# Performance work log

Hardware: AMD Instinct MI355X
Metric: run time of the kernel (lower is better)

The kernel has to match this reference:

```python
import jax, jax.numpy as jnp
import numpy as np

N = 10000
E = 160000
B = 16
NEG_SLOPE = 0.2


def gat_conv(x, src, dst, W, a_src, a_dst, b, heads, ch):
    # x: [N, F_in]; src/dst: [E'] (self-loops included); W: [F_in, heads*ch]
    n = x.shape[0]
    h = (x @ W).reshape(n, heads, ch)                     # [N,H,C]
    alpha_src = jnp.sum(h * a_src, axis=-1)               # [N,H]
    alpha_dst = jnp.sum(h * a_dst, axis=-1)               # [N,H]
    e = jax.nn.leaky_relu(alpha_src[src] + alpha_dst[dst], NEG_SLOPE)  # [E,H]
    # segment softmax over edges grouped by destination node
    m = jax.ops.segment_max(e, dst, num_segments=n)       # [N,H]
    ex = jnp.exp(e - m[dst])                              # [E,H]
    denom = jax.ops.segment_sum(ex, dst, num_segments=n)  # [N,H]
    alpha = ex / denom[dst]                               # [E,H]
    out = jax.ops.segment_sum(alpha[:, :, None] * h[src], dst, num_segments=n)  # [N,H,C]
    return out.reshape(n, heads * ch) + b


def setup_inputs() -> dict:
    key = jax.random.key(0)
    ks = jax.random.split(key, 16)
    glorot = lambda k, shp: jax.random.normal(k, shp, jnp.float32) * np.sqrt(2.0 / (shp[0] + shp[-1]))
    inp = {
        "x": jax.random.normal(ks[0], (N, 128), jnp.float32),
        "edge_index": jax.random.randint(ks[1], (2, E), 0, N, jnp.int64),
        "batch": jnp.sort(jax.random.randint(ks[2], (N,), 0, B, jnp.int64)),
        # conv1: 128 -> 128 per head, 8 heads
        "W1": glorot(ks[3], (128, 8 * 128)),
        "att_src1": glorot(ks[4], (8, 128)),
        "att_dst1": glorot(ks[5], (8, 128)),
        "b1": jnp.zeros((8 * 128,), jnp.float32),
        # conv2: 1024 -> 64 per head, 8 heads
        "W2": glorot(ks[6], (1024, 8 * 64)),
        "att_src2": glorot(ks[7], (8, 64)),
        "att_dst2": glorot(ks[8], (8, 64)),
        "b2": jnp.zeros((8 * 64,), jnp.float32),
        "fc1_w": glorot(ks[9], (512, 32)),
        "fc1_b": jnp.zeros((32,), jnp.float32),
        "fc2_w": glorot(ks[10], (32, 10)),
        "fc2_b": jnp.zeros((10,), jnp.float32),
    }
    return inp


def reference(x, edge_index, batch, W1, att_src1, att_dst1, b1,
              W2, att_src2, att_dst2, b2, fc1_w, fc1_b, fc2_w, fc2_b):
    n = x.shape[0]
    loop = jnp.arange(n, dtype=edge_index.dtype)
    src = jnp.concatenate([edge_index[0], loop])  # PyG add_self_loops=True
    dst = jnp.concatenate([edge_index[1], loop])
    h = jax.nn.elu(gat_conv(x, src, dst, W1, att_src1, att_dst1, b1, 8, 128))   # [N,1024]
    h = jax.nn.elu(gat_conv(h, src, dst, W2, att_src2, att_dst2, b2, 8, 64))    # [N,512]
    # global mean pool over graphs
    sums = jax.ops.segment_sum(h, batch, num_segments=B)                        # [B,512]
    cnt = jax.ops.segment_sum(jnp.ones((n,), h.dtype), batch, num_segments=B)
    g = sums / jnp.maximum(cnt, 1.0)[:, None]
    g = jax.nn.elu(g @ fc1_w + fc1_b)
    return g @ fc2_w + fc2_b                                                    # [B,10]
```

## Files before the change

kernel.cpp:

```cpp
#include <hip/hip_runtime.h>
#include <math.h>

#define HEADS 8
#define NEG 0.2f

typedef unsigned short ushort_t;
typedef __attribute__((ext_vector_type(8))) short short8;
typedef float f32x4 __attribute__((ext_vector_type(4)));

__device__ inline ushort_t f2bf(float f) {
  union { float f; unsigned u; } v; v.f = f;
  unsigned r = (v.u + 0x7FFF + ((v.u >> 16) & 1)) >> 16;
  return (ushort_t)r;
}

__device__ inline float4 bf4(uint2 v) {
  union { unsigned u; float f; } a, b, c, d;
  a.u = v.x << 16; b.u = v.x & 0xffff0000u;
  c.u = v.y << 16; d.u = v.y & 0xffff0000u;
  return make_float4(a.f, b.f, c.f, d.f);
}

__device__ inline float elu_f(float v) {
  return (v > 0.f) ? v : (__expf(v) - 1.f);
}

#define GLDS16(gp, lp)                                                          \
  __builtin_amdgcn_global_load_lds(                                             \
      (const __attribute__((address_space(1))) void*)(gp),                      \
      (__attribute__((address_space(3))) void*)(lp), 16, 0, 0)

__global__ __launch_bounds__(256) void init_k(int* __restrict__ ws, int zero_words,
                                              const float* __restrict__ x,
                                              ushort_t* __restrict__ xb,
                                              const float* __restrict__ W1,
                                              ushort_t* __restrict__ w1t,
                                              const float* __restrict__ W2,
                                              ushort_t* __restrict__ w2t,
                                              const float* __restrict__ as1,
                                              const float* __restrict__ ad1,
                                              float* __restrict__ Ps,
                                              float* __restrict__ Pd, int nx4) {
  __shared__ float tile[32][33];
  int blk = blockIdx.x;
  if (blk < 640) {
    const float* W; ushort_t* Wt; int K, N, tk, tn;
    if (blk < 128) { W = W1; Wt = w1t; K = 128; N = 1024; tk = blk >> 5; tn = blk & 31; }
    else { W = W2; Wt = w2t; K = 1024; N = 512; int t = blk - 128; tk = t >> 4; tn = t & 15; }
    int tx = threadIdx.x & 31, ty = threadIdx.x >> 5;
    int k0 = tk * 32, n0 = tn * 32;
#pragma unroll
    for (int r = 0; r < 4; r++)
      tile[ty + r * 8][tx] = W[(size_t)(k0 + ty + r * 8) * N + n0 + tx];
    __syncthreads();
#pragma unroll
    for (int r = 0; r < 4; r++)
      Wt[(size_t)(n0 + ty + r * 8) * K + k0 + tx] = f2bf(tile[tx][ty + r * 8]);
  } else if (blk < 648) {
    int h = blk - 640;
    int t = threadIdx.x;
    int k = t >> 1, sd = t & 1;
    const float* att = sd ? ad1 : as1;
    float* P = sd ? Pd : Ps;
    const float* wrow = &W1[(size_t)k * 1024 + h * 128];
    const float* arow = &att[h * 128];
    float s = 0.f;
#pragma unroll 8
    for (int c = 0; c < 128; c++) s += wrow[c] * arow[c];
    P[k * 8 + h] = s;
  } else {
    int i = (blk - 648) * 256 + threadIdx.x;
    if (i < zero_words) ws[i] = 0;
    if (i < nx4) {
      float4 v = ((const float4*)x)[i];
      ushort_t o[4] = {f2bf(v.x), f2bf(v.y), f2bf(v.z), f2bf(v.w)};
      *(uint2*)&xb[i * 4] = *(uint2*)o;
    }
  }
}

__global__ void prep_k(const int* __restrict__ ei, int* __restrict__ src,
                       int* __restrict__ dst, int* __restrict__ deg,
                       const int* __restrict__ batch, int* __restrict__ bstart,
                       int* __restrict__ bend, int E, int Nn) {
  int i = blockIdx.x * blockDim.x + threadIdx.x;
  if (i < Nn) {
    int b = batch[i];
    if (i == 0 || batch[i - 1] != b) bstart[b] = i;
    if (i == Nn - 1 || batch[i + 1] != b) bend[b] = i + 1;
  }
  if (i >= E + Nn) return;
  int s, d;
  if (i < E) { s = ei[i]; d = ei[E + i]; }
  else       { s = d = i - E; }
  src[i] = s;
  dst[i] = d;
  atomicAdd(&deg[d], 1);
}

__global__ __launch_bounds__(1024) void scan_k(const int* __restrict__ deg,
                                               int* __restrict__ offs,
                                               int* __restrict__ cursor, int Nn) {
  __shared__ int wtot[16];
  __shared__ int wexcl[16];
  __shared__ int soff_s;
  int t = threadIdx.x;
  int lane = t & 63, w = t >> 6;
  if (t == 0) soff_s = 0;
  __syncthreads();
  for (int base = 0; base < Nn; base += 4096) {
    int idx = base + 4 * t;
    int4 v = make_int4(0, 0, 0, 0);
    if (idx + 3 < Nn) v = *(const int4*)&deg[idx];
    else {
      if (idx < Nn)     v.x = deg[idx];
      if (idx + 1 < Nn) v.y = deg[idx + 1];
      if (idx + 2 < Nn) v.z = deg[idx + 2];
      if (idx + 3 < Nn) v.w = deg[idx + 3];
    }
    int s1 = v.x, s2 = s1 + v.y, s3 = s2 + v.z, s4 = s3 + v.w;
    int sc = s4;
#pragma unroll
    for (int o = 1; o < 64; o <<= 1) {
      int x = __shfl_up(sc, o);
      if (lane >= o) sc += x;
    }
    if (lane == 63) wtot[w] = sc;
    __syncthreads();
    if (w == 0) {
      int tv = (lane < 16) ? wtot[lane] : 0;
      int ts = tv;
#pragma unroll
      for (int o = 1; o < 16; o <<= 1) {
        int x = __shfl_up(ts, o);
        if (lane >= o) ts += x;
      }
      if (lane < 16) wexcl[lane] = ts - tv;
      if (lane == 15) wtot[15] = ts;
    }
    __syncthreads();
    int excl = soff_s + wexcl[w] + (sc - s4);
    int o0 = excl, o1 = excl + s1, o2 = excl + s2, o3 = excl + s3;
    if (idx < Nn)     { offs[idx] = o0;     cursor[idx] = o0; }
    if (idx + 1 < Nn) { offs[idx + 1] = o1; cursor[idx + 1] = o1; }
    if (idx + 2 < Nn) { offs[idx + 2] = o2; cursor[idx + 2] = o2; }
    if (idx + 3 < Nn) { offs[idx + 3] = o3; cursor[idx + 3] = o3; }
    int chunk_total = wtot[15];
    __syncthreads();
    if (t == 0) soff_s += chunk_total;
    __syncthreads();
  }
  if (t == 0) offs[Nn] = soff_s;
}

__global__ __launch_bounds__(256) void scatter_k(const int* __restrict__ src,
                                                 const int* __restrict__ dst,
                                                 int* __restrict__ cursor,
                                                 int* __restrict__ psrc, int Etot, int eb,
                                                 const float* __restrict__ x,
                                                 const float* __restrict__ Ps,
                                                 const float* __restrict__ Pd,
                                                 float* __restrict__ asrc,
                                                 float* __restrict__ adst, int Nn) {
  if ((int)blockIdx.x >= eb) {
    __shared__ float ps[1024], pd[1024];
    int t = threadIdx.x;
    for (int i = t; i < 1024; i += 256) { ps[i] = Ps[i]; pd[i] = Pd[i]; }
    __syncthreads();
    int n = (blockIdx.x - eb) * 256 + t;
    if (n >= Nn) return;
    const float4* xr = (const float4*)&x[(size_t)n * 128];
    float as[8], ad[8];
#pragma unroll
    for (int h = 0; h < 8; h++) { as[h] = 0.f; ad[h] = 0.f; }
    for (int k4 = 0; k4 < 32; k4++) {
      float4 xv = xr[k4];
      float xs[4] = {xv.x, xv.y, xv.z, xv.w};
#pragma unroll
      for (int j = 0; j < 4; j++) {
        int k = k4 * 4 + j;
#pragma unroll
        for (int h = 0; h < 8; h++) {
          as[h] += xs[j] * ps[k * 8 + h];
          ad[h] += xs[j] * pd[k * 8 + h];
        }
      }
    }
#pragma unroll
    for (int h = 0; h < 8; h++) {
      asrc[n * 8 + h] = as[h];
      adst[n * 8 + h] = ad[h];
    }
    return;
  }
  int i = blockIdx.x * 256 + threadIdx.x;
  if (i >= Etot) return;
  int p = atomicAdd(&cursor[dst[i]], 1);
  psrc[p] = src[i];
}

__global__ __launch_bounds__(64) void aggx_k(const ushort_t* __restrict__ xb,
                                             const float* __restrict__ asrc,
                                             const float* __restrict__ adst,
                                             const int* __restrict__ offs,
                                             const int* __restrict__ psrc,
                                             ushort_t* __restrict__ sb, int Nn) {
  int n = blockIdx.x;
  int l = threadIdx.x;
  int u_mine = l >> 3, h_mine = l & 7;
  float adn = adst[n * 8 + h_mine];
  int e0 = offs[n], e1 = offs[n + 1];
  int c0 = l * 2;
  float acc0[8], acc1[8], wsum[8];
#pragma unroll
  for (int h = 0; h < 8; h++) { acc0[h] = 0.f; acc1[h] = 0.f; wsum[h] = 0.f; }

  for (int i = e0; i < e1; i += 8) {
    int bs = min(8, e1 - i);
    int eu = i + (u_mine < bs ? u_mine : bs - 1);
    int se = psrc[eu];
    float v = asrc[se * 8 + h_mine] + adn;
    v = (v > 0.f) ? v : NEG * v;
    float wm = __expf(v);
    int ss[8];
    unsigned xvv[8];
#pragma unroll
    for (int u = 0; u < 8; u++) ss[u] = psrc[i + (u < bs ? u : bs - 1)];
#pragma unroll
    for (int u = 0; u < 8; u++) xvv[u] = *(const unsigned*)&xb[(size_t)ss[u] * 128 + c0];
#pragma unroll
    for (int u = 0; u < 8; u++) {
      if (u < bs) {
        union { unsigned u; float f; } a, b;
        a.u = xvv[u] << 16; b.u = xvv[u] & 0xffff0000u;
#pragma unroll
        for (int h = 0; h < 8; h++) {
          float w = __shfl(wm, (u << 3) | h);
          acc0[h] += w * a.f;
          acc1[h] += w * b.f;
          wsum[h] += w;
        }
      }
    }
  }

#pragma unroll
  for (int h = 0; h < 8; h++) {
    float inv = 1.f / wsum[h];
    unsigned pr = (unsigned)f2bf(acc0[h] * inv) | ((unsigned)f2bf(acc1[h] * inv) << 16);
    *(unsigned*)&sb[(size_t)n * 1024 + h * 128 + c0] = pr;
  }
}

__global__ __launch_bounds__(256) void hgemm_k(const ushort_t* __restrict__ S,
                                               const ushort_t* __restrict__ Wt,
                                               const float* __restrict__ bias,
                                               ushort_t* __restrict__ G, int M) {
  __shared__ __attribute__((aligned(16))) ushort_t lds[32768];
  int tid = threadIdx.x;
  int lane = tid & 63;
  int wave = tid >> 6;
  int wm = (wave >> 1) * 64, wn = (wave & 1) * 64;
  int head = blockIdx.x;
  int hb0 = head * 128;
  int bm = blockIdx.y * 128;
  int lrow = lane & 15, lq = lane >> 4;

  f32x4 acc[4][4];
#pragma unroll
  for (int i = 0; i < 4; i++)
#pragma unroll
    for (int j = 0; j < 4; j++) acc[i][j] = 0.f;

  int srow = lane >> 3;
  int scol = 8 * ((lane & 7) ^ srow);
  const ushort_t* pa[4];
  const ushort_t* pb[4];
  int lofs[4];
#pragma unroll
  for (int c = 0; c < 4; c++) {
    int row = wave * 32 + c * 8 + srow;
    int ga = min(bm + row, M - 1);
    pa[c] = &S[(size_t)ga * 1024 + hb0 + scol];
    pb[c] = &Wt[(size_t)(hb0 + row) * 128 + scol];
    lofs[c] = (wave * 4 + c) * 512;
  }

  auto stage = [&](int buf, int k0) {
#pragma unroll
    for (int c = 0; c < 4; c++) GLDS16(pa[c] + k0, &lds[buf * 8192 + lofs[c]]);
#pragma unroll
    for (int c = 0; c < 4; c++) GLDS16(pb[c] + k0, &lds[16384 + buf * 8192 + lofs[c]]);
  };
  auto compute = [&](int buf) {
    const ushort_t* Asb = &lds[buf * 8192];
    const ushort_t* Bsb = &lds[16384 + buf * 8192];
#pragma unroll
    for (int ks = 0; ks < 2; ks++) {
      short8 af[4], bfr[4];
#pragma unroll
      for (int t = 0; t < 4; t++) {
        int cbs = (ks * 64 + lq * 16) ^ ((lrow & 7) << 4);
        af[t]  = *(const short8*)&Asb[(wm + t * 16 + lrow) * 64 + (cbs >> 1)];
        bfr[t] = *(const short8*)&Bsb[(wn + t * 16 + lrow) * 64 + (cbs >> 1)];
      }
#pragma unroll
      for (int i = 0; i < 4; i++)
#pragma unroll
        for (int j = 0; j < 4; j++)
          acc[i][j] = __builtin_amdgcn_mfma_f32_16x16x32_bf16(af[i], bfr[j], acc[i][j], 0, 0, 0);
    }
  };

  stage(0, 0);
  asm volatile("s_waitcnt vmcnt(0)" ::: "memory");
  __builtin_amdgcn_s_barrier();
  stage(1, 64);
  compute(0);
  asm volatile("s_waitcnt vmcnt(0)" ::: "memory");
  __builtin_amdgcn_s_barrier();
  compute(1);

  __syncthreads();

  ushort_t* Cl = lds;
  float bv[4];
#pragma unroll
  for (int j = 0; j < 4; j++) bv[j] = bias[hb0 + wn + j * 16 + lrow];
#pragma unroll
  for (int i = 0; i < 4; i++) {
#pragma unroll
    for (int j = 0; j < 4; j++) {
      int col = wn + j * 16 + lrow;
#pragma unroll
      for (int r = 0; r < 4; r++) {
        int row = wm + i * 16 + lq * 4 + r;
        Cl[row * 136 + col] = f2bf(elu_f(acc[i][j][r] + bv[j]));
      }
    }
  }
  __syncthreads();
#pragma unroll
  for (int p = 0; p < 8; p++) {
    int row = p * 16 + (tid >> 4);
    int col8 = (tid & 15) * 8;
    if (bm + row < M)
      *(uint4*)&G[(size_t)(bm + row) * 1024 + hb0 + col8] = *(const uint4*)&Cl[row * 136 + col8];
  }
}

__global__ __launch_bounds__(256) void mfma_gemm_k(const ushort_t* __restrict__ A,
                                                   const ushort_t* __restrict__ Bt,
                                                   ushort_t* __restrict__ Cb,
                                                   const float* __restrict__ att_s,
                                                   const float* __restrict__ att_d,
                                                   float* __restrict__ asrc,
                                                   float* __restrict__ adst,
                                                   int M, int N, int K, int CSHIFT) {
  __shared__ __attribute__((aligned(16))) ushort_t lds[24576];
  int tid = threadIdx.x;
  int lane = tid & 63;
  int wave = tid >> 6;
  int wm = (wave >> 1) * 64, wn = (wave & 1) * 32;
  int bm = blockIdx.y * 128, bn = blockIdx.x * 64;
  int lrow = lane & 15, lq = lane >> 4;

  f32x4 acc[4][2];
#pragma unroll
  for (int i = 0; i < 4; i++)
#pragma unroll
    for (int j = 0; j < 2; j++) acc[i][j] = 0.f;

  int srow = lane >> 3;
  int scol = 8 * ((lane & 7) ^ srow);
  const ushort_t* pa[4];
  int laofs[4];
#pragma unroll
  for (int c = 0; c < 4; c++) {
    int row = wave * 32 + c * 8 + srow;
    int ga = min(bm + row, M - 1);
    pa[c] = &A[(size_t)ga * K + scol];
    laofs[c] = (wave * 4 + c) * 512;
  }
  const ushort_t* pb[2];
  int lbofs[2];
#pragma unroll
  for (int c = 0; c < 2; c++) {
    int row = wave * 16 + c * 8 + srow;
    pb[c] = &Bt[(size_t)(bn + row) * K + scol];
    lbofs[c] = (wave * 2 + c) * 512;
  }

  auto stage = [&](int buf, int k0) {
#pragma unroll
    for (int c = 0; c < 4; c++) GLDS16(pa[c] + k0, &lds[buf * 8192 + laofs[c]]);
#pragma unroll
    for (int c = 0; c < 2; c++) GLDS16(pb[c] + k0, &lds[16384 + buf * 4096 + lbofs[c]]);
  };
  auto compute = [&](int buf) {
    const ushort_t* Asb = &lds[buf * 8192];
    const ushort_t* Bsb = &lds[16384 + buf * 4096];
#pragma unroll
    for (int ks = 0; ks < 2; ks++) {
      int cbs = (ks * 64 + lq * 16) ^ ((lrow & 7) << 4);
      short8 af[4], bfr[2];
#pragma unroll
      for (int t = 0; t < 4; t++)
        af[t]  = *(const short8*)&Asb[(wm + t * 16 + lrow) * 64 + (cbs >> 1)];
#pragma unroll
      for (int t = 0; t < 2; t++)
        bfr[t] = *(const short8*)&Bsb[(wn + t * 16 + lrow) * 64 + (cbs >> 1)];
#pragma unroll
      for (int i = 0; i < 4; i++)
#pragma unroll
        for (int j = 0; j < 2; j++)
          acc[i][j] = __builtin_amdgcn_mfma_f32_16x16x32_bf16(af[i], bfr[j], acc[i][j], 0, 0, 0);
    }
  };

  int NT = K >> 6;
  stage(0, 0);
  asm volatile("s_waitcnt vmcnt(0)" ::: "memory");
  __builtin_amdgcn_s_barrier();
  int cur = 0;
  for (int t = 0; t + 1 < NT; ++t) {
    stage(cur ^ 1, (t + 1) << 6);
    compute(cur);
    asm volatile("s_waitcnt vmcnt(0)" ::: "memory");
    __builtin_amdgcn_s_barrier();
    cur ^= 1;
  }
  compute(cur);

  __syncthreads();

  ushort_t* Cl = lds;
  float* pls = (float*)&lds[20480];
  float* pld = pls + 256;

  int hh = bn >> CSHIFT;
  {
    float avs[2], avd[2];
#pragma unroll
    for (int j = 0; j < 2; j++) {
      int col = bn + wn + j * 16 + lrow;
      avs[j] = att_s[col];
      avd[j] = att_d[col];
    }
#pragma unroll
    for (int i = 0; i < 4; i++) {
#pragma unroll
      for (int r = 0; r < 4; r++) {
        float ps = 0.f, pd = 0.f;
#pragma unroll
        for (int j = 0; j < 2; j++) {
          float v = acc[i][j][r];
          ps += v * avs[j];
          pd += v * avd[j];
        }
#pragma unroll
        for (int o = 1; o < 16; o <<= 1) {
          ps += __shfl_xor(ps, o);
          pd += __shfl_xor(pd, o);
        }
        if (lrow == 0) {
          int rr = i * 16 + lq * 4 + r;
          pls[wave * 64 + rr] = ps;
          pld[wave * 64 + rr] = pd;
        }
      }
    }
  }

#pragma unroll
  for (int i = 0; i < 4; i++) {
#pragma unroll
    for (int j = 0; j < 2; j++) {
      int col = wn + j * 16 + lrow;
#pragma unroll
      for (int r = 0; r < 4; r++) {
        int row = wm + i * 16 + lq * 4 + r;
        Cl[row * 72 + col] = f2bf(acc[i][j][r]);
      }
    }
  }
  __syncthreads();

#pragma unroll
  for (int p = 0; p < 4; p++) {
    int row = p * 32 + (tid >> 3);
    int col8 = (tid & 7) * 8;
    if (bm + row < M)
      *(uint4*)&Cb[(size_t)(bm + row) * N + bn + col8] = *(const uint4*)&Cl[row * 72 + col8];
  }

  {
    int r = tid & 127, half = tid >> 7;
    if (bm + r < M) {
      const float* P = half ? pld : pls;
      float* O = half ? adst : asrc;
      int w0 = (r >> 6) * 2, idx = r & 63;
      O[(size_t)(bm + r) * HEADS + hh] = P[w0 * 64 + idx] + P[(w0 + 1) * 64 + idx];
    }
  }
}

template <int F, int CSHIFT, int BT, int NSPLIT, typename OT>
__global__ __launch_bounds__(BT) void aggregate_k(const ushort_t* __restrict__ hb,
                                                  const float* __restrict__ asrc,
                                                  const float* __restrict__ adst,
                                                  const int* __restrict__ offs,
                                                  const int* __restrict__ psrc,
                                                  const float* __restrict__ bias,
                                                  OT* __restrict__ out) {
  constexpr int CPB = F / NSPLIT;
  constexpr int G = (1 << CSHIFT) >> 2;
  static_assert(CPB == 4 * BT, "CPB/thread mismatch");
  static_assert(G >= 8 && G <= 64, "head group must cover the 8-edge batch");
  int nb = blockIdx.x;
  int n = nb / NSPLIT;
  int coff = (nb - n * NSPLIT) * CPB;
  int t = threadIdx.x;
  int c0 = coff + 4 * t;
  int hh = c0 >> CSHIFT;
  int lane = t & 63;
  int sub = lane & (G - 1);
  int gb = lane & ~(G - 1);
  float adn = adst[n * HEADS + hh];
  int e0 = offs[n], e1 = offs[n + 1];
  float4 acc = make_float4(0.f, 0.f, 0.f, 0.f);
  float wsum = 0.f;

  int i = e0;
  uint2 rA[8];
  float myWA = 0.f;
  bool haveA = (i + 8 <= e1);
  if (haveA) {
    int sA[8];
#pragma unroll
    for (int u = 0; u < 8; u++) sA[u] = psrc[i + u];
#pragma unroll
    for (int u = 0; u < 8; u++) rA[u] = *(const uint2*)&hb[(size_t)sA[u] * F + c0];
    int ms = psrc[i + (sub < 8 ? sub : 0)];
    float v = asrc[ms * HEADS + hh] + adn;
    v = (v > 0.f) ? v : NEG * v;
    myWA = __expf(v);
  }
  while (i + 16 <= e1) {
    int sB[8];
    uint2 rB[8];
#pragma unroll
    for (int u = 0; u < 8; u++) sB[u] = psrc[i + 8 + u];
#pragma unroll
    for (int u = 0; u < 8; u++) rB[u] = *(const uint2*)&hb[(size_t)sB[u] * F + c0];
    int ms = psrc[i + 8 + (sub < 8 ? sub : 0)];
    float vb = asrc[ms * HEADS + hh] + adn;
    vb = (vb > 0.f) ? vb : NEG * vb;
    float myWB = __expf(vb);
#pragma unroll
    for (int u = 0; u < 8; u++) {
      float w = __shfl(myWA, gb + u);
      float4 f = bf4(rA[u]);
      wsum += w;
      acc.x += w * f.x;
      acc.y += w * f.y;
      acc.z += w * f.z;
      acc.w += w * f.w;
    }
    i += 8;
#pragma unroll
    for (int u = 0; u < 8; u++) rA[u] = rB[u];
    myWA = myWB;
  }
  if (haveA) {
#pragma unroll
    for (int u = 0; u < 8; u++) {
      float w = __shfl(myWA, gb + u);
      float4 f = bf4(rA[u]);
      wsum += w;
      acc.x += w * f.x;
      acc.y += w * f.y;
      acc.z += w * f.z;
      acc.w += w * f.w;
    }
    i += 8;
  }
  for (; i < e1; i++) {
    int ss = psrc[i];
    float v = asrc[ss * HEADS + hh] + adn;
    v = (v > 0.f) ? v : NEG * v;
    float w = __expf(v);
    float4 f = bf4(*(const uint2*)&hb[(size_t)ss * F + c0]);
    wsum += w;
    acc.x += w * f.x; acc.y += w * f.y;
    acc.z += w * f.z; acc.w += w * f.w;
  }

  float inv = 1.f / wsum;
  float v0 = elu_f(acc.x * inv + bias[c0]);
  float v1 = elu_f(acc.y * inv + bias[c0 + 1]);
  float v2 = elu_f(acc.z * inv + bias[c0 + 2]);
  float v3 = elu_f(acc.w * inv + bias[c0 + 3]);
  if constexpr (sizeof(OT) == 2) {
    unsigned p0 = (unsigned)f2bf(v0) | ((unsigned)f2bf(v1) << 16);
    unsigned p1 = (unsigned)f2bf(v2) | ((unsigned)f2bf(v3) << 16);
    *(uint2*)&((ushort_t*)out)[(size_t)n * F + c0] = make_uint2(p0, p1);
  } else {
    *(float4*)&((float*)out)[(size_t)n * F + c0] = make_float4(v0, v1, v2, v3);
  }
}

__global__ __launch_bounds__(256) void pool_k(const float* __restrict__ g,
                                              const int* __restrict__ batch,
                                              float* __restrict__ sums, int Nn) {
  int c = blockIdx.x * 256 + threadIdx.x;
  int n0 = blockIdx.y * 50;
  int n1 = min(n0 + 50, Nn);
  if (n0 >= n1) return;
  float acc = 0.f;
  int cur = batch[n0];
  for (int n = n0; n < n1; n++) {
    int b = batch[n];
    if (b != cur) { atomicAdd(&sums[cur * 512 + c], acc); acc = 0.f; cur = b; }
    acc += g[(size_t)n * 512 + c];
  }
  atomicAdd(&sums[cur * 512 + c], acc);
}

__global__ __launch_bounds__(512) void mlp_k(const float* __restrict__ sums,
                                             const int* __restrict__ bstart,
                                             const int* __restrict__ bend,
                                             const float* __restrict__ w1,
                                             const float* __restrict__ b1,
                                             const float* __restrict__ w2,
                                             const float* __restrict__ b2,
                                             float* __restrict__ out) {
  __shared__ float gm[16 * 512];
  __shared__ float t1[16 * 32];
  int t = threadIdx.x;
  for (int i = t; i < 16 * 512; i += 512) {
    int b = i >> 9;
    float c = (float)(bend[b] - bstart[b]);
    gm[i] = sums[i] / fmaxf(c, 1.f);
  }
  __syncthreads();
  {
    int b = t >> 5, j = t & 31;
    float s = b1[j];
    for (int k = 0; k < 512; k++) s += gm[(b << 9) + k] * w1[k * 32 + j];
    t1[t] = elu_f(s);
  }
  __syncthreads();
  if (t < 160) {
    int b = t / 10, j = t - b * 10;
    float s = b2[j];
#pragma unroll
    for (int k = 0; k < 32; k++) s += t1[b * 32 + k] * w2[k * 10 + j];
    out[t] = s;
  }
}

extern "C" void kernel_launch(void* const* d_in, const int* in_sizes, int n_in,
                              void* d_out, int out_size, void* d_ws, size_t ws_size,
                              hipStream_t stream) {
  const float* x   = (const float*)d_in[0];
  const int*   ei  = (const int*)d_in[1];
  const int* batch = (const int*)d_in[2];
  const float* W1  = (const float*)d_in[3];
  const float* as1 = (const float*)d_in[4];
  const float* ad1 = (const float*)d_in[5];
  const float* b1  = (const float*)d_in[6];
  const float* W2  = (const float*)d_in[7];
  const float* as2 = (const float*)d_in[8];
  const float* ad2 = (const float*)d_in[9];
  const float* b2  = (const float*)d_in[10];
  const float* f1w = (const float*)d_in[11];
  const float* f1b = (const float*)d_in[12];
  const float* f2w = (const float*)d_in[13];
  const float* f2b = (const float*)d_in[14];
  float* out = (float*)d_out;

  const int Nn = in_sizes[2];
  const int E = in_sizes[1] / 2;
  const int Etot = E + Nn;

  size_t off = 0;
  auto alloc = [&](size_t elems) { size_t o = off; off += (elems + 63) & ~(size_t)63; return o; };
  int* wsi = (int*)d_ws;
  float* wsf = (float*)d_ws;

  size_t o_deg  = alloc(Nn);
  size_t o_pool = alloc(16 * 512);
  size_t zero_words = off;
  size_t o_as1  = alloc((size_t)Nn * 8);
  size_t o_ad1  = alloc((size_t)Nn * 8);
  size_t o_as2  = alloc((size_t)Nn * 8);
  size_t o_ad2  = alloc((size_t)Nn * 8);
  size_t o_ps   = alloc(1024);
  size_t o_pd   = alloc(1024);
  size_t o_bst  = alloc(64);
  size_t o_ben  = alloc(64);
  size_t o_offs = alloc(Nn + 1);
  size_t o_cur  = alloc(Nn);
  size_t o_src  = alloc(Etot);
  size_t o_dst  = alloc(Etot);
  size_t o_psrc = alloc(Etot);
  size_t o_xb   = alloc((size_t)Nn * 128 / 2);
  size_t o_w1t  = alloc(1024 * 128 / 2);
  size_t o_w2t  = alloc(512 * 1024 / 2);
  size_t o_s    = alloc((size_t)Nn * 1024 / 2);
  size_t o_h    = alloc((size_t)Nn * 1024 / 2);
  size_t o_g    = alloc((size_t)Nn * 1024);

  ushort_t* xb  = (ushort_t*)(wsi + o_xb);
  ushort_t* w1t = (ushort_t*)(wsi + o_w1t);
  ushort_t* w2t = (ushort_t*)(wsi + o_w2t);
  ushort_t* sb  = (ushort_t*)(wsi + o_s);
  ushort_t* hb  = (ushort_t*)(wsi + o_h);
  ushort_t* g1b = (ushort_t*)(wsi + o_g);

  int eb = (Etot + 255) / 256;
  int ab = (Nn + 255) / 256;

  int nx4 = Nn * 128 / 4;
  int ep_work = (int)((zero_words > (size_t)nx4 ? zero_words : (size_t)nx4));
  int init_blocks = 648 + (ep_work + 255) / 256;
  init_k<<<init_blocks, 256, 0, stream>>>(wsi, (int)zero_words, x, xb,
                                          W1, w1t, W2, w2t,
                                          as1, ad1, wsf + o_ps, wsf + o_pd, nx4);
  prep_k<<<eb, 256, 0, stream>>>(ei, wsi + o_src, wsi + o_dst, wsi + o_deg,
                                 batch, wsi + o_bst, wsi + o_ben, E, Nn);
  scan_k<<<1, 1024, 0, stream>>>(wsi + o_deg, wsi + o_offs, wsi + o_cur, Nn);
  scatter_k<<<eb + ab, 256, 0, stream>>>(wsi + o_src, wsi + o_dst, wsi + o_cur,
                                         wsi + o_psrc, Etot, eb,
                                         x, wsf + o_ps, wsf + o_pd,
                                         wsf + o_as1, wsf + o_ad1, Nn);

  aggx_k<<<Nn, 64, 0, stream>>>(xb, wsf + o_as1, wsf + o_ad1,
                                wsi + o_offs, wsi + o_psrc, sb, Nn);
  hgemm_k<<<dim3(8, (Nn + 127) / 128), 256, 0, stream>>>(sb, w1t, b1, g1b, Nn);

  mfma_gemm_k<<<dim3(512 / 64, (Nn + 127) / 128), 256, 0, stream>>>(
      g1b, w2t, hb, as2, ad2, wsf + o_as2, wsf + o_ad2, Nn, 512, 1024, 6);
  aggregate_k<512, 6, 64, 2, float><<<Nn * 2, 64, 0, stream>>>(
      hb, wsf + o_as2, wsf + o_ad2, wsi + o_offs, wsi + o_psrc, b2, wsf + o_g);

  pool_k<<<dim3(2, (Nn + 49) / 50), 256, 0, stream>>>(wsf + o_g, batch, wsf + o_pool, Nn);
  mlp_k<<<1, 512, 0, stream>>>(wsf + o_pool, wsi + o_bst, wsi + o_ben, f1w, f1b, f2w, f2b, out);
}
```

Measured before the change: 251.2 us.

## Pack four node-waves per block and double-buffer gathers in aggx

Both aggregation kernels now launch 256-thread blocks in which each of the four waves handles its own node (or node-split unit), replacing one-wave blocks. The aim is to cut block scheduling overhead and keep the GPU fuller with fewer launched blocks. aggx_k also prefetches the next 8-edge batch of source indices, attention weights and feature words while accumulating the current batch, hiding gather latency. The cost is more registers for the second buffer, which may lower occupancy.

```diff
diff --git a/kernel.cpp b/kernel.cpp
--- a/kernel.cpp
+++ b/kernel.cpp
@@ -199,49 +199,67 @@
   psrc[p] = src[i];
 }
 
-__global__ __launch_bounds__(64) void aggx_k(const ushort_t* __restrict__ xb,
-                                             const float* __restrict__ asrc,
-                                             const float* __restrict__ adst,
-                                             const int* __restrict__ offs,
-                                             const int* __restrict__ psrc,
-                                             ushort_t* __restrict__ sb, int Nn) {
-  int n = blockIdx.x;
-  int l = threadIdx.x;
+__global__ __launch_bounds__(256) void aggx_k(const ushort_t* __restrict__ xb,
+                                              const float* __restrict__ asrc,
+                                              const float* __restrict__ adst,
+                                              const int* __restrict__ offs,
+                                              const int* __restrict__ psrc,
+                                              ushort_t* __restrict__ sb, int Nn) {
+  int n = blockIdx.x * 4 + (threadIdx.x >> 6);
+  if (n >= Nn) return;
+  int l = threadIdx.x & 63;
   int u_mine = l >> 3, h_mine = l & 7;
   float adn = adst[n * 8 + h_mine];
   int e0 = offs[n], e1 = offs[n + 1];
   int c0 = l * 2;
+
   float acc0[8], acc1[8], wsum[8];
 #pragma unroll
   for (int h = 0; h < 8; h++) { acc0[h] = 0.f; acc1[h] = 0.f; wsum[h] = 0.f; }
 
-  for (int i = e0; i < e1; i += 8) {
-    int bs = min(8, e1 - i);
-    int eu = i + (u_mine < bs ? u_mine : bs - 1);
+  auto loadb = [&](int ib, int bs, unsigned xv[8], float& wm) {
+    int eu = ib + (u_mine < bs ? u_mine : bs - 1);
     int se = psrc[eu];
     float v = asrc[se * 8 + h_mine] + adn;
     v = (v > 0.f) ? v : NEG * v;
-    float wm = __expf(v);
+    wm = __expf(v);
     int ss[8];
-    unsigned xvv[8];
-#pragma unroll
-    for (int u = 0; u < 8; u++) ss[u] = psrc[i + (u < bs ? u : bs - 1)];
-#pragma unroll
-    for (int u = 0; u < 8; u++) xvv[u] = *(const unsigned*)&xb[(size_t)ss[u] * 128 + c0];
+#pragma unroll
+    for (int u = 0; u < 8; u++) ss[u] = psrc[ib + (u < bs ? u : bs - 1)];
+#pragma unroll
+    for (int u = 0; u < 8; u++) xv[u] = *(const unsigned*)&xb[(size_t)ss[u] * 128 + c0];
+  };
+
+  int i = e0;
+  unsigned xvA[8];
+  float wmA = 0.f;
+  int bsA = 0;
+  if (i < e1) { bsA = min(8, e1 - i); loadb(i, bsA, xvA, wmA); }
+  while (i < e1) {
+    unsigned xvB[8];
+    float wmB = 0.f;
+    int bsB = 0;
+    int inext = i + 8;
+    if (inext < e1) { bsB = min(8, e1 - inext); loadb(inext, bsB, xvB, wmB); }
 #pragma unroll
     for (int u = 0; u < 8; u++) {
-      if (u < bs) {
+      if (u < bsA) {
         union { unsigned u; float f; } a, b;
-        a.u = xvv[u] << 16; b.u = xvv[u] & 0xffff0000u;
+        a.u = xvA[u] << 16; b.u = xvA[u] & 0xffff0000u;
 #pragma unroll
         for (int h = 0; h < 8; h++) {
-          float w = __shfl(wm, (u << 3) | h);
+          float w = __shfl(wmA, (u << 3) | h);
           acc0[h] += w * a.f;
           acc1[h] += w * b.f;
           wsum[h] += w;
         }
       }
     }
+    i = inext;
+    bsA = bsB;
+    wmA = wmB;
+#pragma unroll
+    for (int u = 0; u < 8; u++) xvA[u] = xvB[u];
   }
 
 #pragma unroll
@@ -506,24 +524,26 @@
 }
 
 template <int F, int CSHIFT, int BT, int NSPLIT, typename OT>
-__global__ __launch_bounds__(BT) void aggregate_k(const ushort_t* __restrict__ hb,
-                                                  const float* __restrict__ asrc,
-                                                  const float* __restrict__ adst,
-                                                  const int* __restrict__ offs,
-                                                  const int* __restrict__ psrc,
-                                                  const float* __restrict__ bias,
-                                                  OT* __restrict__ out) {
+__global__ __launch_bounds__(256) void aggregate_k(const ushort_t* __restrict__ hb,
+                                                   const float* __restrict__ asrc,
+                                                   const float* __restrict__ adst,
+                                                   const int* __restrict__ offs,
+                                                   const int* __restrict__ psrc,
+                                                   const float* __restrict__ bias,
+                                                   OT* __restrict__ out, int NU) {
   constexpr int CPB = F / NSPLIT;
   constexpr int G = (1 << CSHIFT) >> 2;
   static_assert(CPB == 4 * BT, "CPB/thread mismatch");
+  static_assert(BT == 64, "unit = one wave");
   static_assert(G >= 8 && G <= 64, "head group must cover the 8-edge batch");
-  int nb = blockIdx.x;
-  int n = nb / NSPLIT;
-  int coff = (nb - n * NSPLIT) * CPB;
-  int t = threadIdx.x;
+  int unit = blockIdx.x * 4 + (threadIdx.x >> 6);
+  if (unit >= NU) return;
+  int n = unit / NSPLIT;
+  int coff = (unit - n * NSPLIT) * CPB;
+  int t = threadIdx.x & 63;
   int c0 = coff + 4 * t;
   int hh = c0 >> CSHIFT;
-  int lane = t & 63;
+  int lane = t;
   int sub = lane & (G - 1);
   int gb = lane & ~(G - 1);
   float adn = adst[n * HEADS + hh];
@@ -736,14 +756,14 @@
                                          x, wsf + o_ps, wsf + o_pd,
                                          wsf + o_as1, wsf + o_ad1, Nn);
 
-  aggx_k<<<Nn, 64, 0, stream>>>(xb, wsf + o_as1, wsf + o_ad1,
-                                wsi + o_offs, wsi + o_psrc, sb, Nn);
+  aggx_k<<<(Nn + 3) / 4, 256, 0, stream>>>(xb, wsf + o_as1, wsf + o_ad1,
+                                           wsi + o_offs, wsi + o_psrc, sb, Nn);
   hgemm_k<<<dim3(8, (Nn + 127) / 128), 256, 0, stream>>>(sb, w1t, b1, g1b, Nn);
 
   mfma_gemm_k<<<dim3(512 / 64, (Nn + 127) / 128), 256, 0, stream>>>(
       g1b, w2t, hb, as2, ad2, wsf + o_as2, wsf + o_ad2, Nn, 512, 1024, 6);
-  aggregate_k<512, 6, 64, 2, float><<<Nn * 2, 64, 0, stream>>>(
-      hb, wsf + o_as2, wsf + o_ad2, wsi + o_offs, wsi + o_psrc, b2, wsf + o_g);
+  aggregate_k<512, 6, 64, 2, float><<<(Nn * 2 + 3) / 4, 256, 0, stream>>>(
+      hb, wsf + o_as2, wsf + o_ad2, wsi + o_offs, wsi + o_psrc, b2, wsf + o_g, Nn * 2);
 
   pool_k<<<dim3(2, (Nn + 49) / 50), 256, 0, stream>>>(wsf + o_g, batch, wsf + o_pool, Nn);
   mlp_k<<<1, 512, 0, stream>>>(wsf + o_pool, wsi + o_bst, wsi + o_ben, f1w, f1b, f2w, f2b, out);
```

Result: slower. 261.7 us (+4.2%).
